# Kernel tuning notes

Measured on AMD Instinct MI355X. Metric: run time of the kernel, lower is better.

The kernel has to match this reference:

```python
import jax, jax.numpy as jnp
import numpy as np

FD, NH, SP, GS = 256, 4, 2, 80.0
E = FD // NH
SP3 = SP ** 3


def _bilinear(plane, uv):
    # plane: [B,C,H,W], uv: [B,N,2] in [0,1] -> [B,C,N] (align_corners=True style)
    B, C, H, W = plane.shape
    x = jnp.clip(uv[..., 0], 0.0, 1.0) * (W - 1)
    y = jnp.clip(uv[..., 1], 0.0, 1.0) * (H - 1)
    x0 = jnp.floor(x); y0 = jnp.floor(y)
    wx = (x - x0)[:, None, :]; wy = (y - y0)[:, None, :]
    x0i = x0.astype(jnp.int32); y0i = y0.astype(jnp.int32)
    x1i = jnp.minimum(x0i + 1, W - 1); y1i = jnp.minimum(y0i + 1, H - 1)
    g = jax.vmap(lambda pl, yy, xx: pl[:, yy, xx])  # per-batch gather -> [C,N]
    f00 = g(plane, y0i, x0i); f01 = g(plane, y0i, x1i)
    f10 = g(plane, y1i, x0i); f11 = g(plane, y1i, x1i)
    return (f00 * (1 - wy) * (1 - wx) + f01 * (1 - wy) * wx
            + f10 * wy * (1 - wx) + f11 * wy * wx)


def _triplane(p, c_xz, c_xy, c_yz):
    # p: [B,N,3] in [0,1] -> [B,N,FD]; sum of three plane samples (ConvONet style)
    px, py, pz = p[..., 0], p[..., 1], p[..., 2]
    f = (_bilinear(c_xz, jnp.stack([px, pz], -1))
         + _bilinear(c_xy, jnp.stack([px, py], -1))
         + _bilinear(c_yz, jnp.stack([py, pz], -1)))
    return jnp.swapaxes(f, 1, 2)


def setup_inputs() -> dict:
    key = jax.random.key(0)
    ks = jax.random.split(key, 10)
    bs, ns, H = 4, 1024, 128
    inp = {}
    inp['query_pos'] = jax.random.uniform(ks[0], (bs, ns, 3), dtype=jnp.float32)
    for i, nm in enumerate(['c_xz', 'c_xy', 'c_yz']):
        inp[nm] = jax.random.normal(ks[1 + i], (bs, FD, H, H), dtype=jnp.float32)

    def lin(k, fi, fo):  # xavier-uniform like torch init
        lim = (6.0 / (fi + fo)) ** 0.5
        return jax.random.uniform(k, (fi, fo), minval=-lim, maxval=lim, dtype=jnp.float32)

    # to_offset: small random weight (torch inits to 0; small noise exercises the path),
    # bias = normalized sp^3 anchor grid / grid_scale, tiled over heads (as in __init__)
    inp['w_off'] = 0.01 * jax.random.normal(ks[4], (FD, SP3 * NH * 3), dtype=jnp.float32)
    g = np.stack(np.meshgrid(np.arange(SP), np.arange(SP), np.arange(SP), indexing='ij'), axis=-1).astype(np.float32)
    gsc = (2.0 * g / max(SP - 1, 1) - 1.0) / GS  # [sp,sp,sp,3]
    inp['b_off'] = jnp.asarray(np.tile(gsc[:, :, :, None, :], (1, 1, 1, NH, 1)).reshape(-1))
    inp['w_q'] = lin(ks[5], FD, E); inp['b_q'] = jnp.zeros((E,), jnp.float32)
    inp['w_k'] = lin(ks[6], FD, E); inp['b_k'] = jnp.zeros((E,), jnp.float32)
    inp['w_v'] = lin(ks[7], FD, E); inp['b_v'] = jnp.zeros((E,), jnp.float32)
    inp['w_out'] = lin(ks[8], FD, FD); inp['b_out'] = jnp.zeros((FD,), jnp.float32)
    return inp


def reference(query_pos, c_xz, c_xy, c_yz, w_off, b_off, w_q, b_q, w_k, b_k, w_v, b_v, w_out, b_out):
    bs, ns, _ = query_pos.shape
    feature = _triplane(query_pos, c_xz, c_xy, c_yz)                 # [bs,ns,FD]
    off = (feature @ w_off + b_off).reshape(bs, ns, SP3, NH, 3)
    aux = off + query_pos[:, :, None, None, :]                        # [bs,ns,SP3,NH,3]
    aux_feat = _triplane(aux.reshape(bs, -1, 3), c_xz, c_xy, c_yz)
    aux_feat = aux_feat.reshape(bs * ns, SP3, NH, FD)
    k = jnp.swapaxes(aux_feat @ w_k + b_k, 1, 2)                      # [bn,NH,SP3,E]
    v = jnp.swapaxes(aux_feat @ w_v + b_v, 1, 2)
    # note: original does q / scale with scale = E**-0.5, i.e. q * sqrt(E)
    q = (feature @ w_q + b_q).reshape(bs * ns, 1, 1, E) * (E ** 0.5)
    q = jnp.broadcast_to(q, (bs * ns, NH, 1, E))
    sim = jnp.einsum('bnid,bnjd->bnij', q, k)                         # [bn,NH,1,SP3]
    attn = jax.nn.softmax(sim, axis=-1)                               # dropout = identity (eval)
    out = jnp.einsum('bnij,bnjd->bnid', attn, v)                      # [bn,NH,1,E]
    out = jnp.swapaxes(out, 1, 2).reshape(bs, ns, NH * E)
    return out @ w_out + b_out + feature
```

## Files before the change

### kernel.cpp

```cpp
#include <hip/hip_runtime.h>
#include <math.h>

#define FD   256
#define NH   4
#define SP3  8
#define NP   32
#define EDIM 64
#define H    128
#define NS   1024
#define BS   4
#define QT   8

#define TEX         (H*H)
#define BATCH_ELEMS (TEX*FD)
#define PAIR_B      2
#define PAIR_Q      (PAIR_B*NS)
#define PPLANE      (PAIR_B*BATCH_ELEMS)

#define WS_PLANES 0
#define WS_FEAT   (3*PPLANE)
#define WS_QK     (WS_FEAT + PAIR_Q*FD)
#define WS_AUX    (WS_QK   + PAIR_Q*FD)
#define WS_WF     (WS_AUX  + PAIR_Q*NP*3)
#define WS_PERM   (WS_WF   + PAIR_Q*NH*FD)

__global__ __launch_bounds__(256) void tpk2(
    const float* __restrict__ xz, const float* __restrict__ xy,
    const float* __restrict__ yz, float* __restrict__ dstAll, int b0)
{
  int bid = blockIdx.x;
  int tT = bid & 255; bid >>= 8;
  int bl = bid & 1;   bid >>= 1;
  int pl = bid;
  const float* src = pl == 0 ? xz : (pl == 1 ? xy : yz);
  float* dst = dstAll + (size_t)pl * PPLANE + (size_t)bl * BATCH_ELEMS;
  int b = b0 + bl;

  __shared__ float T[64 * 260];
  int lane = threadIdx.x & 63, w = threadIdx.x >> 6;
  int lrow = lane >> 4;
  int ltex = (lane & 15) << 2;

  const float* sbase = src + (size_t)b * FD * TEX + tT * 64;
  #pragma unroll
  for (int i = 0; i < 16; i++) {
    int c = i * 16 + w * 4 + lrow;
    float4 v = *(const float4*)(sbase + (size_t)c * TEX + ltex);
    T[(ltex + 0) * 260 + c] = v.x;
    T[(ltex + 1) * 260 + c] = v.y;
    T[(ltex + 2) * 260 + c] = v.z;
    T[(ltex + 3) * 260 + c] = v.w;
  }
  __syncthreads();
  #pragma unroll
  for (int i = 0; i < 16; i++) {
    int t = w * 16 + i;
    float4 v = *(const float4*)(&T[t * 260 + lane * 4]);
    *(float4*)(dst + (size_t)(tT * 64 + t) * FD + lane * 4) = v;
  }
}

__device__ __forceinline__ unsigned mort7(unsigned v) {
  unsigned r = 0;
  #pragma unroll
  for (int i = 0; i < 7; i++) r |= ((v >> i) & 1u) << (3 * i);
  return r;
}

__global__ __launch_bounds__(1024) void sortk(
    const float* __restrict__ qpos, unsigned* __restrict__ perm)
{
  const int pair = blockIdx.x;
  const int b0 = pair * PAIR_B;
  const int t = threadIdx.x;
  __shared__ unsigned long long s_kv[PAIR_Q];

  for (int i = t; i < PAIR_Q; i += 1024) {
    size_t qg = (size_t)b0 * NS + i;
    float x = fminf(fmaxf(qpos[qg * 3 + 0], 0.f), 1.f);
    float y = fminf(fmaxf(qpos[qg * 3 + 1], 0.f), 1.f);
    float z = fminf(fmaxf(qpos[qg * 3 + 2], 0.f), 1.f);
    unsigned xi = (unsigned)(x * 127.0f);
    unsigned yi = (unsigned)(y * 127.0f);
    unsigned zi = (unsigned)(z * 127.0f);
    unsigned key = ((unsigned)(i >> 10) << 21)
                 | (mort7(xi) << 2) | (mort7(yi) << 1) | mort7(zi);
    s_kv[i] = ((unsigned long long)key << 32) | (unsigned)i;
  }
  for (unsigned k = 2; k <= PAIR_Q; k <<= 1) {
    for (unsigned j = k >> 1; j > 0; j >>= 1) {
      __syncthreads();
      for (int i = t; i < PAIR_Q; i += 1024) {
        int ixj = i ^ (int)j;
        if (ixj > i) {
          unsigned long long a = s_kv[i], b = s_kv[ixj];
          bool asc = ((i & (int)k) == 0);
          if ((a > b) == asc) { s_kv[i] = b; s_kv[ixj] = a; }
        }
      }
    }
  }
  __syncthreads();
  for (int i = t; i < PAIR_Q; i += 1024)
    perm[(size_t)pair * PAIR_Q + i] = (unsigned)(s_kv[i] & 0xFFFFFFFFu);
}

__device__ __forceinline__ float sample_plane(const float* __restrict__ p,
                                              float u, float v) {
  float x = fminf(fmaxf(u, 0.f), 1.f) * (float)(H - 1);
  float y = fminf(fmaxf(v, 0.f), 1.f) * (float)(H - 1);
  float xf = floorf(x), yf = floorf(y);
  int x0 = (int)xf, y0 = (int)yf;
  float wx = x - xf, wy = y - yf;
  int dx = (x0 < H - 1) ? FD : 0;
  int dy = (y0 < H - 1) ? H * FD : 0;
  int i00 = (y0 * H + x0) * FD;
  float f00 = p[i00], f01 = p[i00 + dx], f10 = p[i00 + dy], f11 = p[i00 + dy + dx];
  float a = f00 + wx * (f01 - f00);
  float b = f10 + wx * (f11 - f10);
  return a + wy * (b - a);
}

__device__ __forceinline__ void setup_samp(int* si, float* sw, float u, float v) {
  float x = fminf(fmaxf(u, 0.f), 1.f) * (float)(H - 1);
  float y = fminf(fmaxf(v, 0.f), 1.f) * (float)(H - 1);
  float xf = floorf(x), yf = floorf(y);
  int x0 = (int)xf, y0 = (int)yf;
  float wx = x - xf, wy = y - yf;
  si[0] = (y0 * H + x0) * FD;
  si[1] = (x0 < H - 1) ? FD : 0;
  si[2] = (y0 < H - 1) ? H * FD : 0;
  sw[0] = (1.f - wy) * (1.f - wx);
  sw[1] = (1.f - wy) * wx;
  sw[2] = wy * (1.f - wx);
  sw[3] = wy * wx;
}

__global__ __launch_bounds__(256) void featk(
    const float* __restrict__ qpos, const float* __restrict__ planesT,
    const float* __restrict__ w_off, const float* __restrict__ b_off,
    const float* __restrict__ w_q, const float* __restrict__ b_q,
    const float* __restrict__ w_k,
    float* __restrict__ feat, float* __restrict__ aux, float* __restrict__ qk,
    int b0)
{
  const int tid = threadIdx.x;
  const int q0l = blockIdx.x * QT;
  const int bl = q0l >> 10;
  __shared__ float s_feat[QT * 260];
  __shared__ float s_q[QT * 68];

  const float* Pxz = planesT + 0 * (size_t)PPLANE + (size_t)bl * BATCH_ELEMS + tid;
  const float* Pxy = planesT + 1 * (size_t)PPLANE + (size_t)bl * BATCH_ELEMS + tid;
  const float* Pyz = planesT + 2 * (size_t)PPLANE + (size_t)bl * BATCH_ELEMS + tid;

  for (int qs = 0; qs < QT; qs++) {
    size_t qg = (size_t)b0 * NS + q0l + qs;
    float px = qpos[qg * 3 + 0], py = qpos[qg * 3 + 1], pz = qpos[qg * 3 + 2];
    float f = sample_plane(Pxz, px, pz) + sample_plane(Pxy, px, py)
            + sample_plane(Pyz, py, pz);
    s_feat[qs * 260 + tid] = f;
    feat[(size_t)(q0l + qs) * FD + tid] = f;
  }
  __syncthreads();

  if (tid < 192) {
    int half = tid / 96, j = tid - half * 96;
    float acc[4];
    float bj = b_off[j];
    #pragma unroll
    for (int k = 0; k < 4; k++) acc[k] = bj;
    for (int c = 0; c < FD; c++) {
      float wv = w_off[c * 96 + j];
      #pragma unroll
      for (int k = 0; k < 4; k++)
        acc[k] = fmaf(s_feat[(half * 4 + k) * 260 + c], wv, acc[k]);
    }
    int d = j % 3;
    #pragma unroll
    for (int k = 0; k < 4; k++) {
      int qs = half * 4 + k;
      size_t qg = (size_t)b0 * NS + q0l + qs;
      aux[(size_t)(q0l + qs) * 96 + j] = acc[k] + qpos[qg * 3 + d];
    }
  }
  {
    int e = tid & 63, g = tid >> 6;
    #pragma unroll
    for (int k = 0; k < 2; k++) {
      int qs = g * 2 + k;
      float a = b_q[e];
      for (int c = 0; c < FD; c++)
        a = fmaf(s_feat[qs * 260 + c], w_q[c * EDIM + e], a);
      s_q[qs * 68 + e] = a * 8.0f;
    }
  }
  __syncthreads();
  {
    float acc[QT];
    #pragma unroll
    for (int qs = 0; qs < QT; qs++) acc[qs] = 0.f;
    const float4* wk4 = reinterpret_cast<const float4*>(w_k + (size_t)tid * EDIM);
    for (int e4 = 0; e4 < EDIM / 4; e4++) {
      float4 wv = wk4[e4];
      int e = e4 * 4;
      #pragma unroll
      for (int qs = 0; qs < QT; qs++) {
        acc[qs] = fmaf(s_q[qs * 68 + e + 0], wv.x, acc[qs]);
        acc[qs] = fmaf(s_q[qs * 68 + e + 1], wv.y, acc[qs]);
        acc[qs] = fmaf(s_q[qs * 68 + e + 2], wv.z, acc[qs]);
        acc[qs] = fmaf(s_q[qs * 68 + e + 3], wv.w, acc[qs]);
      }
    }
    #pragma unroll
    for (int qs = 0; qs < QT; qs++)
      qk[(size_t)(q0l + qs) * FD + tid] = acc[qs];
  }
}

__global__ __launch_bounds__(256) void attnk(
    const float* __restrict__ planesT, const float* __restrict__ aux,
    const float* __restrict__ qk, const unsigned* __restrict__ perm,
    float* __restrict__ wf)
{
  const int tid = threadIdx.x, lane = tid & 63, w = tid >> 6;
  const int bid = blockIdx.x;
  const int q = (int)perm[((bid & 7) << 8) | (bid >> 3)];
  const int bl = q >> 10;
  const int c4 = lane * 4;

  __shared__ int   s_si[96][3];
  __shared__ float s_sw[96][4];
  __shared__ float s_sim[NP];
  __shared__ float s_attn[NP];
  __shared__ float4 s_af[NP * 64];

  const float* P0 = planesT + 0 * (size_t)PPLANE + (size_t)bl * BATCH_ELEMS + c4;
  const float* P1 = planesT + 1 * (size_t)PPLANE + (size_t)bl * BATCH_ELEMS + c4;
  const float* P2 = planesT + 2 * (size_t)PPLANE + (size_t)bl * BATCH_ELEMS + c4;

  if (tid < 96) {
    int p = tid / 3, pl = tid - p * 3;
    float ax = aux[(size_t)q * 96 + p * 3 + 0];
    float ay = aux[(size_t)q * 96 + p * 3 + 1];
    float az = aux[(size_t)q * 96 + p * 3 + 2];
    float u = (pl == 2) ? ay : ax;
    float v = (pl == 1) ? ay : az;
    setup_samp(s_si[tid], s_sw[tid], u, v);
  }
  float4 qk4 = *(const float4*)(qk + (size_t)q * FD + c4);
  __syncthreads();

  #pragma unroll 2
  for (int k = 0; k < 8; k++) {
    int p = w * 8 + k;
    float4 a; a.x = 0.f; a.y = 0.f; a.z = 0.f; a.w = 0.f;
    #pragma unroll
    for (int pl = 0; pl < 3; pl++) {
      const float* P = pl == 0 ? P0 : (pl == 1 ? P1 : P2);
      int i00 = s_si[p * 3 + pl][0];
      int dxo = s_si[p * 3 + pl][1];
      int dyo = s_si[p * 3 + pl][2];
      float w0 = s_sw[p * 3 + pl][0], w1 = s_sw[p * 3 + pl][1];
      float w2 = s_sw[p * 3 + pl][2], w3 = s_sw[p * 3 + pl][3];
      float4 f00 = *(const float4*)(P + i00);
      float4 f01 = *(const float4*)(P + i00 + dxo);
      float4 f10 = *(const float4*)(P + i00 + dyo);
      float4 f11 = *(const float4*)(P + i00 + dyo + dxo);
      a.x = fmaf(w0, f00.x, fmaf(w1, f01.x, fmaf(w2, f10.x, fmaf(w3, f11.x, a.x))));
      a.y = fmaf(w0, f00.y, fmaf(w1, f01.y, fmaf(w2, f10.y, fmaf(w3, f11.y, a.y))));
      a.z = fmaf(w0, f00.z, fmaf(w1, f01.z, fmaf(w2, f10.z, fmaf(w3, f11.z, a.z))));
      a.w = fmaf(w0, f00.w, fmaf(w1, f01.w, fmaf(w2, f10.w, fmaf(w3, f11.w, a.w))));
    }
    s_af[p * 64 + lane] = a;
    float t = fmaf(qk4.x, a.x, fmaf(qk4.y, a.y, fmaf(qk4.z, a.z, qk4.w * a.w)));
    #pragma unroll
    for (int o = 32; o >= 1; o >>= 1) t += __shfl_xor(t, o, 64);
    if (lane == 0) s_sim[p] = t;
  }
  __syncthreads();

  if (tid < NH) {
    float sim[SP3], m = -1e30f;
    #pragma unroll
    for (int j = 0; j < SP3; j++) { sim[j] = s_sim[j * NH + tid]; m = fmaxf(m, sim[j]); }
    float sum = 0.f, e_[SP3];
    #pragma unroll
    for (int j = 0; j < SP3; j++) { e_[j] = __expf(sim[j] - m); sum += e_[j]; }
    float inv = 1.0f / sum;
    #pragma unroll
    for (int j = 0; j < SP3; j++) s_attn[j * NH + tid] = e_[j] * inv;
  }
  __syncthreads();

  {
    float4 r; r.x = 0.f; r.y = 0.f; r.z = 0.f; r.w = 0.f;
    #pragma unroll
    for (int j = 0; j < SP3; j++) {
      int p = j * NH + w;
      float a = s_attn[p];
      float4 f = s_af[p * 64 + lane];
      r.x = fmaf(a, f.x, r.x);
      r.y = fmaf(a, f.y, r.y);
      r.z = fmaf(a, f.z, r.z);
      r.w = fmaf(a, f.w, r.w);
    }
    *(float4*)(wf + ((size_t)q * NH + w) * FD + c4) = r;
  }
}

__global__ __launch_bounds__(256) void epik(
    const float* __restrict__ wf, const float* __restrict__ feat,
    const float* __restrict__ w_v, const float* __restrict__ b_v,
    const float* __restrict__ w_out, const float* __restrict__ b_out,
    float* __restrict__ out, int b0)
{
  const int tid = threadIdx.x;
  const int q0l = blockIdx.x * QT;
  __shared__ float s_wv[FD * EDIM];
  __shared__ float s_o[QT * 257];

  {
    const float4* src4 = (const float4*)w_v;
    float4* dst4 = (float4*)s_wv;
    #pragma unroll
    for (int i = 0; i < (FD * EDIM / 4) / 256; i++)
      dst4[tid + 256 * i] = src4[tid + 256 * i];
  }
  __syncthreads();

  {
    int h = tid >> 6, e = tid & 63;
    float acc[QT];
    float bv = b_v[e];
    #pragma unroll
    for (int qs = 0; qs < QT; qs++) acc[qs] = bv;
    const float* wrow = wf + ((size_t)q0l * NH + h) * FD;
    for (int c = 0; c < FD; c++) {
      float wv = s_wv[c * EDIM + e];
      #pragma unroll
      for (int qs = 0; qs < QT; qs++)
        acc[qs] = fmaf(wrow[(size_t)qs * NH * FD + c], wv, acc[qs]);
    }
    #pragma unroll
    for (int qs = 0; qs < QT; qs++) s_o[qs * 257 + h * EDIM + e] = acc[qs];
  }
  __syncthreads();

  {
    float r[QT];
    float bo = b_out[tid];
    #pragma unroll
    for (int qs = 0; qs < QT; qs++) r[qs] = bo;
    for (int c = 0; c < FD; c++) {
      float wv = w_out[(size_t)c * FD + tid];
      #pragma unroll
      for (int qs = 0; qs < QT; qs++)
        r[qs] = fmaf(s_o[qs * 257 + c], wv, r[qs]);
    }
    #pragma unroll
    for (int qs = 0; qs < QT; qs++)
      out[((size_t)b0 * NS + q0l + qs) * FD + tid]
          = r[qs] + feat[(size_t)(q0l + qs) * FD + tid];
  }
}

extern "C" void kernel_launch(void* const* d_in, const int* in_sizes, int n_in,
                              void* d_out, int out_size, void* d_ws, size_t ws_size,
                              hipStream_t stream) {
  const float* qp    = (const float*)d_in[0];
  const float* cxz   = (const float*)d_in[1];
  const float* cxy   = (const float*)d_in[2];
  const float* cyz   = (const float*)d_in[3];
  const float* w_off = (const float*)d_in[4];
  const float* b_off = (const float*)d_in[5];
  const float* w_q   = (const float*)d_in[6];
  const float* b_q   = (const float*)d_in[7];
  const float* w_k   = (const float*)d_in[8];
  const float* b_k   = (const float*)d_in[9];   (void)b_k;
  const float* w_v   = (const float*)d_in[10];
  const float* b_v   = (const float*)d_in[11];
  const float* w_out = (const float*)d_in[12];
  const float* b_out = (const float*)d_in[13];
  float* out = (float*)d_out;
  (void)in_sizes; (void)n_in; (void)out_size; (void)ws_size;

  float* ws      = (float*)d_ws;
  float* planesT = ws + WS_PLANES;
  float* feat    = ws + WS_FEAT;
  float* qk      = ws + WS_QK;
  float* aux     = ws + WS_AUX;
  float* wf      = ws + WS_WF;
  unsigned* perm = (unsigned*)(ws + WS_PERM);

  hipLaunchKernelGGL(sortk, dim3(BS / PAIR_B), dim3(1024), 0, stream, qp, perm);

  for (int pair = 0; pair < BS / PAIR_B; ++pair) {
    int b0 = pair * PAIR_B;
    hipLaunchKernelGGL(tpk2, dim3(3 * PAIR_B * 256), dim3(256), 0, stream,
                       cxz, cxy, cyz, planesT, b0);
    hipLaunchKernelGGL(featk, dim3(PAIR_Q / QT), dim3(256), 0, stream,
                       qp, planesT, w_off, b_off, w_q, b_q, w_k,
                       feat, aux, qk, b0);
    hipLaunchKernelGGL(attnk, dim3(PAIR_Q), dim3(256), 0, stream,
                       planesT, aux, qk, perm + (size_t)pair * PAIR_Q, wf);
    hipLaunchKernelGGL(epik, dim3(PAIR_Q / QT), dim3(256), 0, stream,
                       wf, feat, w_v, b_v, w_out, b_out, out, b0);
  }
}
```

Measured before the change: 552.9 us.

## Bucket-sort queries, process two queries per attention block, store features in bf16

Replaces the full bitonic Morton sort with a single-pass 256-bucket counting sort on the top Morton bits. The attention kernel now handles two queries per block, and the sampled aux features are stored in shared memory as bf16 to halve LDS use. The transpose kernel uses 32-texel tiles, which doubles its grid and halves its shared memory. These changes aim to cut sort cost and raise occupancy, at the cost of coarser spatial ordering and some precision loss in the attention-weighted sum.

```diff
diff --git a/kernel.cpp b/kernel.cpp
--- a/kernel.cpp
+++ b/kernel.cpp
@@ -24,39 +24,47 @@
 #define WS_WF     (WS_AUX  + PAIR_Q*NP*3)
 #define WS_PERM   (WS_WF   + PAIR_Q*NH*FD)
 
+__device__ __forceinline__ unsigned short f2bf(float f) {
+  unsigned b = __float_as_uint(f);
+  return (unsigned short)((b + 0x7FFFu + ((b >> 16) & 1u)) >> 16);
+}
+__device__ __forceinline__ float bf2f(unsigned short u) {
+  return __uint_as_float(((unsigned)u) << 16);
+}
+
 __global__ __launch_bounds__(256) void tpk2(
     const float* __restrict__ xz, const float* __restrict__ xy,
     const float* __restrict__ yz, float* __restrict__ dstAll, int b0)
 {
   int bid = blockIdx.x;
-  int tT = bid & 255; bid >>= 8;
+  int tT = bid & 511; bid >>= 9;
   int bl = bid & 1;   bid >>= 1;
   int pl = bid;
   const float* src = pl == 0 ? xz : (pl == 1 ? xy : yz);
   float* dst = dstAll + (size_t)pl * PPLANE + (size_t)bl * BATCH_ELEMS;
   int b = b0 + bl;
 
-  __shared__ float T[64 * 260];
+  __shared__ float T[32 * 260];
   int lane = threadIdx.x & 63, w = threadIdx.x >> 6;
-  int lrow = lane >> 4;
-  int ltex = (lane & 15) << 2;
-
-  const float* sbase = src + (size_t)b * FD * TEX + tT * 64;
+  int tex4 = (lane & 7) * 4;
+  int csub = lane >> 3;
+
+  const float* sbase = src + (size_t)b * FD * TEX + tT * 32;
   #pragma unroll
-  for (int i = 0; i < 16; i++) {
-    int c = i * 16 + w * 4 + lrow;
-    float4 v = *(const float4*)(sbase + (size_t)c * TEX + ltex);
-    T[(ltex + 0) * 260 + c] = v.x;
-    T[(ltex + 1) * 260 + c] = v.y;
-    T[(ltex + 2) * 260 + c] = v.z;
-    T[(ltex + 3) * 260 + c] = v.w;
+  for (int i = 0; i < 8; i++) {
+    int c = i * 32 + w * 8 + csub;
+    float4 v = *(const float4*)(sbase + (size_t)c * TEX + tex4);
+    T[(tex4 + 0) * 260 + c] = v.x;
+    T[(tex4 + 1) * 260 + c] = v.y;
+    T[(tex4 + 2) * 260 + c] = v.z;
+    T[(tex4 + 3) * 260 + c] = v.w;
   }
   __syncthreads();
   #pragma unroll
-  for (int i = 0; i < 16; i++) {
-    int t = w * 16 + i;
+  for (int i = 0; i < 8; i++) {
+    int t = w * 8 + i;
     float4 v = *(const float4*)(&T[t * 260 + lane * 4]);
-    *(float4*)(dst + (size_t)(tT * 64 + t) * FD + lane * 4) = v;
+    *(float4*)(dst + (size_t)(tT * 32 + t) * FD + lane * 4) = v;
   }
 }
 
@@ -73,36 +81,37 @@
   const int pair = blockIdx.x;
   const int b0 = pair * PAIR_B;
   const int t = threadIdx.x;
-  __shared__ unsigned long long s_kv[PAIR_Q];
-
-  for (int i = t; i < PAIR_Q; i += 1024) {
+  __shared__ unsigned cnt[256];
+  __shared__ unsigned base[256];
+  if (t < 256) cnt[t] = 0;
+  __syncthreads();
+  unsigned myb[2];
+  #pragma unroll
+  for (int r = 0; r < 2; r++) {
+    int i = t + r * 1024;
     size_t qg = (size_t)b0 * NS + i;
     float x = fminf(fmaxf(qpos[qg * 3 + 0], 0.f), 1.f);
     float y = fminf(fmaxf(qpos[qg * 3 + 1], 0.f), 1.f);
     float z = fminf(fmaxf(qpos[qg * 3 + 2], 0.f), 1.f);
-    unsigned xi = (unsigned)(x * 127.0f);
-    unsigned yi = (unsigned)(y * 127.0f);
-    unsigned zi = (unsigned)(z * 127.0f);
-    unsigned key = ((unsigned)(i >> 10) << 21)
-                 | (mort7(xi) << 2) | (mort7(yi) << 1) | mort7(zi);
-    s_kv[i] = ((unsigned long long)key << 32) | (unsigned)i;
-  }
-  for (unsigned k = 2; k <= PAIR_Q; k <<= 1) {
-    for (unsigned j = k >> 1; j > 0; j >>= 1) {
-      __syncthreads();
-      for (int i = t; i < PAIR_Q; i += 1024) {
-        int ixj = i ^ (int)j;
-        if (ixj > i) {
-          unsigned long long a = s_kv[i], b = s_kv[ixj];
-          bool asc = ((i & (int)k) == 0);
-          if ((a > b) == asc) { s_kv[i] = b; s_kv[ixj] = a; }
-        }
-      }
-    }
-  }
-  __syncthreads();
-  for (int i = t; i < PAIR_Q; i += 1024)
-    perm[(size_t)pair * PAIR_Q + i] = (unsigned)(s_kv[i] & 0xFFFFFFFFu);
+    unsigned m = (mort7((unsigned)(x * 127.f)) << 2)
+               | (mort7((unsigned)(y * 127.f)) << 1)
+               |  mort7((unsigned)(z * 127.f));
+    unsigned bkt = ((unsigned)(i >> 10) << 7) | (m >> 14);
+    myb[r] = bkt;
+    atomicAdd(&cnt[bkt], 1u);
+  }
+  __syncthreads();
+  if (t == 0) {
+    unsigned s = 0;
+    for (int k = 0; k < 256; k++) { base[k] = s; s += cnt[k]; }
+  }
+  __syncthreads();
+  #pragma unroll
+  for (int r = 0; r < 2; r++) {
+    int i = t + r * 1024;
+    unsigned pos = atomicAdd(&base[myb[r]], 1u);
+    perm[(size_t)pair * PAIR_Q + pos] = (unsigned)i;
+  }
 }
 
 __device__ __forceinline__ float sample_plane(const float* __restrict__ p,
@@ -225,44 +234,51 @@
 {
   const int tid = threadIdx.x, lane = tid & 63, w = tid >> 6;
   const int bid = blockIdx.x;
-  const int q = (int)perm[((bid & 7) << 8) | (bid >> 3)];
-  const int bl = q >> 10;
+  const int j = ((bid & 7) << 7) | (bid >> 3);
   const int c4 = lane * 4;
 
-  __shared__ int   s_si[96][3];
-  __shared__ float s_sw[96][4];
-  __shared__ float s_sim[NP];
-  __shared__ float s_attn[NP];
-  __shared__ float4 s_af[NP * 64];
-
-  const float* P0 = planesT + 0 * (size_t)PPLANE + (size_t)bl * BATCH_ELEMS + c4;
-  const float* P1 = planesT + 1 * (size_t)PPLANE + (size_t)bl * BATCH_ELEMS + c4;
-  const float* P2 = planesT + 2 * (size_t)PPLANE + (size_t)bl * BATCH_ELEMS + c4;
-
-  if (tid < 96) {
-    int p = tid / 3, pl = tid - p * 3;
-    float ax = aux[(size_t)q * 96 + p * 3 + 0];
-    float ay = aux[(size_t)q * 96 + p * 3 + 1];
-    float az = aux[(size_t)q * 96 + p * 3 + 2];
+  __shared__ int     s_si[2][96][3];
+  __shared__ float   s_sw[2][96][4];
+  __shared__ float   s_sim[2][NP];
+  __shared__ float   s_attn[2][NP];
+  __shared__ ushort4 s_af[2 * NP * 64];
+  __shared__ int     s_q[2];
+
+  if (tid < 2) s_q[tid] = (int)perm[2 * j + tid];
+  __syncthreads();
+  const int qw = s_q[w >> 1];
+  const int blw = qw >> 10;
+
+  if (tid < 192) {
+    int qi = tid / 96, r = tid - qi * 96;
+    int p = r / 3, pl = r - p * 3;
+    int qq = s_q[qi];
+    float ax = aux[(size_t)qq * 96 + p * 3 + 0];
+    float ay = aux[(size_t)qq * 96 + p * 3 + 1];
+    float az = aux[(size_t)qq * 96 + p * 3 + 2];
     float u = (pl == 2) ? ay : ax;
     float v = (pl == 1) ? ay : az;
-    setup_samp(s_si[tid], s_sw[tid], u, v);
-  }
-  float4 qk4 = *(const float4*)(qk + (size_t)q * FD + c4);
-  __syncthreads();
-
+    setup_samp(s_si[qi][r], s_sw[qi][r], u, v);
+  }
+  float4 qk4 = *(const float4*)(qk + (size_t)qw * FD + c4);
+  const float* P0 = planesT + 0 * (size_t)PPLANE + (size_t)blw * BATCH_ELEMS + c4;
+  const float* P1 = planesT + 1 * (size_t)PPLANE + (size_t)blw * BATCH_ELEMS + c4;
+  const float* P2 = planesT + 2 * (size_t)PPLANE + (size_t)blw * BATCH_ELEMS + c4;
+  __syncthreads();
+
+  const int qi = w >> 1;
   #pragma unroll 2
-  for (int k = 0; k < 8; k++) {
-    int p = w * 8 + k;
+  for (int k = 0; k < 16; k++) {
+    int p = (w & 1) * 16 + k;
     float4 a; a.x = 0.f; a.y = 0.f; a.z = 0.f; a.w = 0.f;
     #pragma unroll
     for (int pl = 0; pl < 3; pl++) {
       const float* P = pl == 0 ? P0 : (pl == 1 ? P1 : P2);
-      int i00 = s_si[p * 3 + pl][0];
-      int dxo = s_si[p * 3 + pl][1];
-      int dyo = s_si[p * 3 + pl][2];
-      float w0 = s_sw[p * 3 + pl][0], w1 = s_sw[p * 3 + pl][1];
-      float w2 = s_sw[p * 3 + pl][2], w3 = s_sw[p * 3 + pl][3];
+      int i00 = s_si[qi][p * 3 + pl][0];
+      int dxo = s_si[qi][p * 3 + pl][1];
+      int dyo = s_si[qi][p * 3 + pl][2];
+      float w0 = s_sw[qi][p * 3 + pl][0], w1 = s_sw[qi][p * 3 + pl][1];
+      float w2 = s_sw[qi][p * 3 + pl][2], w3 = s_sw[qi][p * 3 + pl][3];
       float4 f00 = *(const float4*)(P + i00);
       float4 f01 = *(const float4*)(P + i00 + dxo);
       float4 f10 = *(const float4*)(P + i00 + dyo);
@@ -272,40 +288,47 @@
       a.z = fmaf(w0, f00.z, fmaf(w1, f01.z, fmaf(w2, f10.z, fmaf(w3, f11.z, a.z))));
       a.w = fmaf(w0, f00.w, fmaf(w1, f01.w, fmaf(w2, f10.w, fmaf(w3, f11.w, a.w))));
     }
-    s_af[p * 64 + lane] = a;
+    ushort4 h;
+    h.x = f2bf(a.x); h.y = f2bf(a.y); h.z = f2bf(a.z); h.w = f2bf(a.w);
+    s_af[(qi * NP + p) * 64 + lane] = h;
     float t = fmaf(qk4.x, a.x, fmaf(qk4.y, a.y, fmaf(qk4.z, a.z, qk4.w * a.w)));
     #pragma unroll
     for (int o = 32; o >= 1; o >>= 1) t += __shfl_xor(t, o, 64);
-    if (lane == 0) s_sim[p] = t;
-  }
-  __syncthreads();
-
-  if (tid < NH) {
+    if (lane == 0) s_sim[qi][p] = t;
+  }
+  __syncthreads();
+
+  if (tid < 2 * NH) {
+    int si = tid >> 2, h = tid & 3;
     float sim[SP3], m = -1e30f;
     #pragma unroll
-    for (int j = 0; j < SP3; j++) { sim[j] = s_sim[j * NH + tid]; m = fmaxf(m, sim[j]); }
+    for (int jj = 0; jj < SP3; jj++) { sim[jj] = s_sim[si][jj * NH + h]; m = fmaxf(m, sim[jj]); }
     float sum = 0.f, e_[SP3];
     #pragma unroll
-    for (int j = 0; j < SP3; j++) { e_[j] = __expf(sim[j] - m); sum += e_[j]; }
+    for (int jj = 0; jj < SP3; jj++) { e_[jj] = __expf(sim[jj] - m); sum += e_[jj]; }
     float inv = 1.0f / sum;
     #pragma unroll
-    for (int j = 0; j < SP3; j++) s_attn[j * NH + tid] = e_[j] * inv;
-  }
-  __syncthreads();
-
-  {
-    float4 r; r.x = 0.f; r.y = 0.f; r.z = 0.f; r.w = 0.f;
-    #pragma unroll
-    for (int j = 0; j < SP3; j++) {
-      int p = j * NH + w;
-      float a = s_attn[p];
-      float4 f = s_af[p * 64 + lane];
-      r.x = fmaf(a, f.x, r.x);
-      r.y = fmaf(a, f.y, r.y);
-      r.z = fmaf(a, f.z, r.z);
-      r.w = fmaf(a, f.w, r.w);
-    }
-    *(float4*)(wf + ((size_t)q * NH + w) * FD + c4) = r;
+    for (int jj = 0; jj < SP3; jj++) s_attn[si][jj * NH + h] = e_[jj] * inv;
+  }
+  __syncthreads();
+
+  {
+    #pragma unroll
+    for (int hi = 0; hi < 2; hi++) {
+      int h = (w & 1) + hi * 2;
+      float4 r; r.x = 0.f; r.y = 0.f; r.z = 0.f; r.w = 0.f;
+      #pragma unroll
+      for (int jj = 0; jj < SP3; jj++) {
+        int p = jj * NH + h;
+        float a = s_attn[qi][p];
+        ushort4 hv = s_af[(qi * NP + p) * 64 + lane];
+        r.x = fmaf(a, bf2f(hv.x), r.x);
+        r.y = fmaf(a, bf2f(hv.y), r.y);
+        r.z = fmaf(a, bf2f(hv.z), r.z);
+        r.w = fmaf(a, bf2f(hv.w), r.w);
+      }
+      *(float4*)(wf + ((size_t)qw * NH + h) * FD + c4) = r;
+    }
   }
 }
 
@@ -397,12 +420,12 @@
 
   for (int pair = 0; pair < BS / PAIR_B; ++pair) {
     int b0 = pair * PAIR_B;
-    hipLaunchKernelGGL(tpk2, dim3(3 * PAIR_B * 256), dim3(256), 0, stream,
+    hipLaunchKernelGGL(tpk2, dim3(3 * PAIR_B * 512), dim3(256), 0, stream,
                        cxz, cxy, cyz, planesT, b0);
     hipLaunchKernelGGL(featk, dim3(PAIR_Q / QT), dim3(256), 0, stream,
                        qp, planesT, w_off, b_off, w_q, b_q, w_k,
                        feat, aux, qk, b0);
-    hipLaunchKernelGGL(attnk, dim3(PAIR_Q), dim3(256), 0, stream,
+    hipLaunchKernelGGL(attnk, dim3(PAIR_Q / 2), dim3(256), 0, stream,
                        planesT, aux, qk, perm + (size_t)pair * PAIR_Q, wf);
     hipLaunchKernelGGL(epik, dim3(PAIR_Q / QT), dim3(256), 0, stream,
                        wf, feat, w_v, b_v, w_out, b_out, out, b0);
```

Measured after the change: 540.5 us. -2.2%, faster.
